# Performance work log

Hardware: AMD Instinct MI355X
Metric: run time of the kernel (lower is better)

## Reference

```python
import jax, jax.numpy as jnp
import numpy as np

COMMITMENT_COST = 0.25
ENTROPY_WEIGHT = 0.1
EPS = 1e-10


def setup_inputs() -> dict:
    key = jax.random.key(0)
    k1, k2 = jax.random.split(key)
    B, L, D, K = 8, 4096, 256, 4096
    z = jax.random.normal(k1, (B, L, D), dtype=jnp.float32)
    # torch init: uniform(-1/K, 1/K)
    codebook_weight = jax.random.uniform(k2, (K, D), dtype=jnp.float32,
                                         minval=-1.0 / K, maxval=1.0 / K)
    return {"z": z, "codebook_weight": codebook_weight}


def reference(z, codebook_weight):
    B, L, D = z.shape
    z_flat = z.reshape(-1, D)                       # [N, D]
    # squared euclidean distances: [N, K]
    d2 = (jnp.sum(z_flat ** 2, axis=1, keepdims=True)
          + jnp.sum(codebook_weight ** 2, axis=1)
          - 2.0 * z_flat @ codebook_weight.T)
    indices = jnp.argmin(d2, axis=1)                # [N]
    z_q_flat = codebook_weight[indices]             # gather [N, D]
    z_q = z_q_flat.reshape(B, L, D)

    codebook_loss = jnp.mean((z_q - jax.lax.stop_gradient(z)) ** 2)
    commitment_loss = jnp.mean((jax.lax.stop_gradient(z_q) - z) ** 2)

    probs = jax.nn.softmax(-d2, axis=1)             # [N, K]
    avg_probs = probs.mean(axis=0)                  # [K]
    entropy = -jnp.sum(avg_probs * jnp.log(avg_probs + EPS))
    entropy_loss = -entropy

    codebook_commitment_loss = codebook_loss + COMMITMENT_COST * commitment_loss
    scaled_entropy_loss = ENTROPY_WEIGHT * entropy_loss
    vq_loss = codebook_commitment_loss + scaled_entropy_loss

    # straight-through estimator
    z_q_ste = z + jax.lax.stop_gradient(z_q - z)
    indices_out = indices.reshape(B, L)
    return (z_q_ste, indices_out, vq_loss, codebook_commitment_loss, scaled_entropy_loss)
```

## Files before the change

### kernel.cpp

```cpp
#include <hip/hip_runtime.h>
#include <stdint.h>

#define NROWS 32768
#define KC 4096
#define DIM 256
#define BM 32
#define NCT 128
#define NWV 8
#define TPW 16
#define CAP 40
#define KAPPA 0.99960f
#define K2L2E 2.88539008f
#define L2E 1.44269504f

#define OUT_IDX (NROWS * DIM)
#define OUT_SCAL (OUT_IDX + NROWS)

#define WS_CNORM 0
#define WS_ZNORM 16384
#define WS_LOSS  147456
#define WS_AVGP8 147712
#define WS_FRAG  278784

typedef __bf16 bf8 __attribute__((ext_vector_type(8)));
typedef float f16v __attribute__((ext_vector_type(16)));

__device__ __forceinline__ unsigned ford(float f) {
  unsigned u = __float_as_uint(f);
  return (u & 0x80000000u) ? ~u : (u | 0x80000000u);
}

__device__ __forceinline__ float np_rownorm256(const float* __restrict__ p) {
  float h[2];
  #pragma unroll
  for (int half = 0; half < 2; ++half) {
    const float* b = p + half * 128;
    float r[8];
    #pragma unroll
    for (int j = 0; j < 8; ++j) { float v = b[j]; r[j] = __fmul_rn(v, v); }
    for (int i = 8; i < 128; i += 8) {
      #pragma unroll
      for (int j = 0; j < 8; ++j) {
        float v = b[i + j];
        r[j] = __fadd_rn(r[j], __fmul_rn(v, v));
      }
    }
    h[half] = __fadd_rn(
        __fadd_rn(__fadd_rn(r[0], r[1]), __fadd_rn(r[2], r[3])),
        __fadd_rn(__fadd_rn(r[4], r[5]), __fadd_rn(r[6], r[7])));
  }
  return __fadd_rn(h[0], h[1]);
}

__global__ void k_norms(const float* __restrict__ cbw, const float* __restrict__ z,
                        float* __restrict__ cnorm, float* __restrict__ znorm) {
  int r = blockIdx.x * 256 + threadIdx.x;
  if (r < KC) cnorm[r] = np_rownorm256(cbw + (size_t)r * DIM);
  else {
    int q = r - KC;
    if (q < NROWS) znorm[q] = np_rownorm256(z + (size_t)q * DIM);
  }
}

__global__ void k_frag(const float* __restrict__ cbw, __bf16* __restrict__ frag) {
  int idx = blockIdx.x * 256 + threadIdx.x;
  int c = idx >> 5, u = idx & 31;
  int ds = u >> 1, half = u & 1;
  int ct = c >> 5, m = c & 31;
  int lane = half * 32 + m;
  const float* src = cbw + (size_t)c * DIM + ds * 16 + half * 8;
  float4 a = *(const float4*)src;
  float4 b = *(const float4*)(src + 4);
  bf8 h;
  h[0] = (__bf16)a.x; h[1] = (__bf16)a.y; h[2] = (__bf16)a.z; h[3] = (__bf16)a.w;
  h[4] = (__bf16)b.x; h[5] = (__bf16)b.y; h[6] = (__bf16)b.z; h[7] = (__bf16)b.w;
  *(bf8*)(frag + ((size_t)(ct * 16 + ds) * 64 + lane) * 8) = h;
}

__device__ __forceinline__ float exact_d2(const float* __restrict__ zr,
                                          const float* __restrict__ cr,
                                          float rn, float cn) {
  float mm = 0.f;
  for (int d = 0; d < DIM; d += 4) {
    float4 zv = *(const float4*)(zr + d);
    float4 cv = *(const float4*)(cr + d);
    mm = __builtin_fmaf(zv.x, cv.x, mm);
    mm = __builtin_fmaf(zv.y, cv.y, mm);
    mm = __builtin_fmaf(zv.z, cv.z, mm);
    mm = __builtin_fmaf(zv.w, cv.w, mm);
  }
  return __fsub_rn(__fadd_rn(rn, cn), __fmul_rn(2.f, mm));
}

__device__ __forceinline__ void tile_mfma(const __bf16* __restrict__ Aimg,
                                          const __bf16* __restrict__ tb,
                                          int lane, f16v& acc) {
  #pragma unroll
  for (int r = 0; r < 16; ++r) acc[r] = 0.f;
  #pragma unroll
  for (int ds = 0; ds < 16; ++ds) {
    bf8 Bf = *(const bf8*)(tb + (ds * 64 + lane) * 8);
    bf8 Af = *(const bf8*)&Aimg[((size_t)ds * 64 + lane) * 8];
    acc = __builtin_amdgcn_mfma_f32_32x32x16_bf16(Af, Bf, acc, 0, 0, 0);
  }
}

__global__ __launch_bounds__(512, 4) void k_main(
    const float* __restrict__ z, const float* __restrict__ cbw,
    const float* __restrict__ cnorm, const float* __restrict__ znorm,
    const __bf16* __restrict__ frag, float* __restrict__ out,
    float* __restrict__ avgp8, double* __restrict__ losssum) {
  __shared__ __bf16 Aimg[16 * 64 * 8];
  union CP { int cand[BM][CAP]; float pcol[KC]; };
  __shared__ CP cp;
  __shared__ int ccount[BM];
  __shared__ unsigned rowmaxU[BM];
  __shared__ unsigned long long rowkey[BM];
  __shared__ float esumL[BM], invR[BM], lred[512];
  __shared__ int idxr[BM];

  const int t = threadIdx.x;
  const int lane = t & 63, wv = t >> 6;
  const int ln31 = lane & 31, lh = lane >> 5;
  const int row0 = blockIdx.x * BM;

  if (t < BM) {
    ccount[t] = 0; rowmaxU[t] = 0u; rowkey[t] = ~0ULL; esumL[t] = 0.f;
  }

  #pragma unroll
  for (int i = 0; i < 2; ++i) {
    int idx = t * 2 + i;
    int l = idx & 63, ds = idx >> 6;
    int row = l & 31, d0 = ds * 16 + (l >> 5) * 8;
    const float* src = z + (size_t)(row0 + row) * DIM + d0;
    float4 a = *(const float4*)src;
    float4 b = *(const float4*)(src + 4);
    bf8 h;
    h[0] = (__bf16)a.x; h[1] = (__bf16)a.y; h[2] = (__bf16)a.z; h[3] = (__bf16)a.w;
    h[4] = (__bf16)b.x; h[5] = (__bf16)b.y; h[6] = (__bf16)b.z; h[7] = (__bf16)b.w;
    *(bf8*)&Aimg[((size_t)ds * 64 + l) * 8] = h;
  }
  __syncthreads();

  const int ctbase = wv * TPW;

  {
    f16v acc;
    tile_mfma(Aimg, frag + (size_t)ctbase * 8192, lane, acc);
    const float cnl = cnorm[ctbase * 32 + ln31] * L2E;
    #pragma unroll
    for (int r = 0; r < 16; ++r) {
      const int row = (r & 3) + 8 * (r >> 2) + 4 * lh;
      float e = exp2f(__builtin_fmaf(acc[r], K2L2E, -cnl));
      atomicMax(&rowmaxU[row], __float_as_uint(e));
    }
  }
  __syncthreads();

  float es[16];
  #pragma unroll
  for (int i = 0; i < 16; ++i) es[i] = 0.f;

  for (int ti = 0; ti < TPW; ++ti) {
    const int ct = ctbase + ti;
    const float cnl = cnorm[ct * 32 + ln31] * L2E;

    float cr[16];
    {
      const float4* rmf = (const float4*)rowmaxU;
      float4 c0 = rmf[lh], c1 = rmf[2 + lh], c2 = rmf[4 + lh], c3 = rmf[6 + lh];
      cr[0]  = c0.x; cr[1]  = c0.y; cr[2]  = c0.z; cr[3]  = c0.w;
      cr[4]  = c1.x; cr[5]  = c1.y; cr[6]  = c1.z; cr[7]  = c1.w;
      cr[8]  = c2.x; cr[9]  = c2.y; cr[10] = c2.z; cr[11] = c2.w;
      cr[12] = c3.x; cr[13] = c3.y; cr[14] = c3.z; cr[15] = c3.w;
    }

    f16v acc;
    tile_mfma(Aimg, frag + (size_t)ct * 8192, lane, acc);

    unsigned cond = 0u;
    #pragma unroll
    for (int r = 0; r < 16; ++r) {
      float e = exp2f(__builtin_fmaf(acc[r], K2L2E, -cnl));
      es[r] += e;
      cond |= (e >= cr[r] * KAPPA) ? (1u << r) : 0u;
    }
    if (cond) {
      #pragma unroll
      for (int r = 0; r < 16; ++r) {
        if (cond & (1u << r)) {
          const int row = (r & 3) + 8 * (r >> 2) + 4 * lh;
          float e = exp2f(__builtin_fmaf(acc[r], K2L2E, -cnl));
          atomicMax(&rowmaxU[row], __float_as_uint(e));
          int slot = atomicAdd(&ccount[row], 1);
          if (slot < CAP) cp.cand[row][slot] = ct * 32 + ln31;
        }
      }
    }
  }

  #pragma unroll
  for (int r = 0; r < 16; ++r) {
    float e = es[r];
    #pragma unroll
    for (int off = 16; off > 0; off >>= 1) e += __shfl_xor(e, off);
    if (ln31 == 0) {
      const int row = (r & 3) + 8 * (r >> 2) + 4 * lh;
      atomicAdd(&esumL[row], e);
    }
  }
  __syncthreads();
  if (t < BM) invR[t] = 1.0f / esumL[t];
  __syncthreads();

  {
    int r = t & 31, q = t >> 5;
    int cnt = ccount[r];
    const float* zr = z + (size_t)(row0 + r) * DIM;
    float rn = znorm[row0 + r];
    if (cnt <= CAP) {
      for (int s = q; s < cnt; s += 16) {
        int k = cp.cand[r][s];
        float d2 = exact_d2(zr, cbw + (size_t)k * DIM, rn, cnorm[k]);
        atomicMin(&rowkey[r], (((unsigned long long)ford(d2)) << 32) | (unsigned)k);
      }
    } else {
      for (int k = q; k < KC; k += 16) {
        float d2 = exact_d2(zr, cbw + (size_t)k * DIM, rn, cnorm[k]);
        atomicMin(&rowkey[r], (((unsigned long long)ford(d2)) << 32) | (unsigned)k);
      }
    }
  }
  __syncthreads();
  if (t < BM) {
    int idx = (int)(rowkey[t] & 0xFFFFFFFFULL);
    idxr[t] = idx;
    out[OUT_IDX + row0 + t] = (float)idx;
  }
  __syncthreads();

  float lacc = 0.f;
  {
    const int col = t & 255;
    for (int r = (t >> 8); r < BM; r += 2) {
      int idx = idxr[r];
      float zq = cbw[(size_t)idx * DIM + col];
      float zv = z[(size_t)(row0 + r) * DIM + col];
      float df = __fsub_rn(zq, zv);
      out[(size_t)(row0 + r) * DIM + col] = __fadd_rn(zv, df);
      lacc += df * df;
    }
  }
  lred[t] = lacc;
  __syncthreads();
  #pragma unroll
  for (int s = 256; s > 0; s >>= 1) {
    if (t < s) lred[t] += lred[t + s];
    __syncthreads();
  }
  if (t == 0) atomicAdd(losssum, (double)lred[0]);

  float ir[16];
  #pragma unroll
  for (int r = 0; r < 16; ++r)
    ir[r] = invR[(r & 3) + 8 * (r >> 2) + 4 * lh];
  __syncthreads();

  for (int ti = 0; ti < TPW; ++ti) {
    const int ct = ctbase + ti;
    f16v acc;
    tile_mfma(Aimg, frag + (size_t)ct * 8192, lane, acc);
    const float cnl = cnorm[ct * 32 + ln31] * L2E;
    float s = 0.f;
    #pragma unroll
    for (int r = 0; r < 16; ++r) {
      float e = exp2f(__builtin_fmaf(acc[r], K2L2E, -cnl));
      s = __builtin_fmaf(e, ir[r], s);
    }
    s += __shfl_xor(s, 32);
    if (lh == 0) cp.pcol[ct * 32 + ln31] = s;
  }
  __syncthreads();
  {
    float* shadow = avgp8 + (size_t)(blockIdx.x & 7) * KC;
    #pragma unroll
    for (int i = 0; i < 8; ++i)
      atomicAdd(&shadow[t + 512 * i], cp.pcol[t + 512 * i]);
  }
}

__global__ void k_final(const float* __restrict__ avgp8,
                        const double* __restrict__ losssum,
                        float* __restrict__ out) {
  const int t = threadIdx.x;
  double part = 0.0;
  for (int k = t; k < KC; k += 256) {
    float a4 = 0.f;
    #pragma unroll
    for (int s = 0; s < 8; ++s) a4 += avgp8[s * KC + k];
    double a = (double)a4 / (double)NROWS;
    part += a * log(a + 1e-10);
  }
  __shared__ double sd[256];
  sd[t] = part;
  __syncthreads();
  for (int s = 128; s > 0; s >>= 1) {
    if (t < s) sd[t] += sd[t + s];
    __syncthreads();
  }
  if (t == 0) {
    double H = -sd[0];
    double mse = losssum[0] / (double)((size_t)NROWS * DIM);
    double ccl = 1.25 * mse;
    double sel = -0.1 * H;
    out[OUT_SCAL + 0] = (float)(ccl + sel);
    out[OUT_SCAL + 1] = (float)ccl;
    out[OUT_SCAL + 2] = (float)sel;
  }
}

extern "C" void kernel_launch(void* const* d_in, const int* in_sizes, int n_in,
                              void* d_out, int out_size, void* d_ws, size_t ws_size,
                              hipStream_t stream) {
  const float* z = (const float*)d_in[0];
  const float* cbw = (const float*)d_in[1];
  float* out = (float*)d_out;
  char* ws = (char*)d_ws;
  float* cnorm = (float*)(ws + WS_CNORM);
  float* znorm = (float*)(ws + WS_ZNORM);
  double* losssum = (double*)(ws + WS_LOSS);
  float* avgp8 = (float*)(ws + WS_AVGP8);
  __bf16* frag = (__bf16*)(ws + WS_FRAG);

  hipMemsetAsync(ws + WS_LOSS, 0, 8, stream);
  hipMemsetAsync(ws + WS_AVGP8, 0, 8 * KC * 4, stream);
  k_norms<<<(KC + NROWS) / 256, 256, 0, stream>>>(cbw, z, cnorm, znorm);
  k_frag<<<(KC * 32) / 256, 256, 0, stream>>>(cbw, frag);
  k_main<<<NROWS / BM, 512, 0, stream>>>(z, cbw, cnorm, znorm, frag, out,
                                         avgp8, losssum);
  k_final<<<1, 256, 0, stream>>>(avgp8, losssum, out);
}
```

Measured before the change: 464.5 us.

## Double-buffer codebook fragments into LDS via global_load_lds in both MFMA passes

Replaces direct global loads of B fragments inside the MFMA loops with a double-buffered LDS staging pipeline, using async global-to-LDS copies one half-tile ahead. Both the argmin/softmax-sum pass and the probability pass now run 34/32-step loops with a block-wide barrier each step. The second pass writes its column sums straight to the global shadow array with atomics instead of going through a shared buffer. The new 128KB of LDS staging forces launch bounds down from 4 to 2 blocks per CU, and the per-step barriers add synchronisation cost.

New measurement: 582.7 us. 1.25x slower.

```diff
diff --git a/kernel.cpp b/kernel.cpp
--- a/kernel.cpp
+++ b/kernel.cpp
@@ -24,6 +24,11 @@
 
 typedef __bf16 bf8 __attribute__((ext_vector_type(8)));
 typedef float f16v __attribute__((ext_vector_type(16)));
+
+#define GLOAD_LDS(g, l) \
+  __builtin_amdgcn_global_load_lds( \
+      (const __attribute__((address_space(1))) void*)(g), \
+      (__attribute__((address_space(3))) void*)(l), 16, 0, 0)
 
 __device__ __forceinline__ unsigned ford(float f) {
   unsigned u = __float_as_uint(f);
@@ -92,27 +97,24 @@
   return __fsub_rn(__fadd_rn(rn, cn), __fmul_rn(2.f, mm));
 }
 
-__device__ __forceinline__ void tile_mfma(const __bf16* __restrict__ Aimg,
-                                          const __bf16* __restrict__ tb,
-                                          int lane, f16v& acc) {
-  #pragma unroll
-  for (int r = 0; r < 16; ++r) acc[r] = 0.f;
-  #pragma unroll
-  for (int ds = 0; ds < 16; ++ds) {
-    bf8 Bf = *(const bf8*)(tb + (ds * 64 + lane) * 8);
-    bf8 Af = *(const bf8*)&Aimg[((size_t)ds * 64 + lane) * 8];
-    acc = __builtin_amdgcn_mfma_f32_32x32x16_bf16(Af, Bf, acc, 0, 0, 0);
-  }
-}
-
-__global__ __launch_bounds__(512, 4) void k_main(
+__device__ __forceinline__ void stage_half(const __bf16* __restrict__ frag,
+                                           __bf16* dst, int ct, int h, int lane) {
+  const char* g = (const char*)frag + (size_t)ct * 16384 + (size_t)h * 8192
+                  + (size_t)lane * 16;
+  char* l = (char*)dst;
+  #pragma unroll
+  for (int c = 0; c < 8; ++c)
+    GLOAD_LDS(g + c * 1024, l + c * 1024);
+}
+
+__global__ __launch_bounds__(512, 2) void k_main(
     const float* __restrict__ z, const float* __restrict__ cbw,
     const float* __restrict__ cnorm, const float* __restrict__ znorm,
     const __bf16* __restrict__ frag, float* __restrict__ out,
     float* __restrict__ avgp8, double* __restrict__ losssum) {
-  __shared__ __bf16 Aimg[16 * 64 * 8];
-  union CP { int cand[BM][CAP]; float pcol[KC]; };
-  __shared__ CP cp;
+  __shared__ __attribute__((aligned(16))) __bf16 Aimg[16 * 64 * 8];
+  __shared__ __attribute__((aligned(16))) __bf16 Bst[2][NWV][4096];
+  __shared__ int cand[BM][CAP];
   __shared__ int ccount[BM];
   __shared__ unsigned rowmaxU[BM];
   __shared__ unsigned long long rowkey[BM];
@@ -145,58 +147,77 @@
 
   const int ctbase = wv * TPW;
 
+  float es[16];
+  #pragma unroll
+  for (int i = 0; i < 16; ++i) es[i] = 0.f;
+
+#define CONSUME_HALF(bufptr, hh)                                              \
+  {                                                                           \
+    const __bf16* bs_ = (bufptr);                                             \
+    _Pragma("unroll")                                                         \
+    for (int c_ = 0; c_ < 8; ++c_) {                                          \
+      bf8 Bf = *(const bf8*)(bs_ + c_ * 512 + lane * 8);                      \
+      bf8 Af = *(const bf8*)&Aimg[((size_t)((hh) * 8 + c_) * 64 + lane) * 8]; \
+      acc = __builtin_amdgcn_mfma_f32_32x32x16_bf16(Af, Bf, acc, 0, 0, 0);    \
+    }                                                                         \
+  }
+
   {
+    stage_half(frag, &Bst[0][wv][0], ctbase, 0, lane);
+    __syncthreads();
+
+    float cr[16];
     f16v acc;
-    tile_mfma(Aimg, frag + (size_t)ctbase * 8192, lane, acc);
-    const float cnl = cnorm[ctbase * 32 + ln31] * L2E;
-    #pragma unroll
-    for (int r = 0; r < 16; ++r) {
-      const int row = (r & 3) + 8 * (r >> 2) + 4 * lh;
-      float e = exp2f(__builtin_fmaf(acc[r], K2L2E, -cnl));
-      atomicMax(&rowmaxU[row], __float_as_uint(e));
-    }
-  }
-  __syncthreads();
-
-  float es[16];
-  #pragma unroll
-  for (int i = 0; i < 16; ++i) es[i] = 0.f;
-
-  for (int ti = 0; ti < TPW; ++ti) {
-    const int ct = ctbase + ti;
-    const float cnl = cnorm[ct * 32 + ln31] * L2E;
-
-    float cr[16];
-    {
-      const float4* rmf = (const float4*)rowmaxU;
-      float4 c0 = rmf[lh], c1 = rmf[2 + lh], c2 = rmf[4 + lh], c3 = rmf[6 + lh];
-      cr[0]  = c0.x; cr[1]  = c0.y; cr[2]  = c0.z; cr[3]  = c0.w;
-      cr[4]  = c1.x; cr[5]  = c1.y; cr[6]  = c1.z; cr[7]  = c1.w;
-      cr[8]  = c2.x; cr[9]  = c2.y; cr[10] = c2.z; cr[11] = c2.w;
-      cr[12] = c3.x; cr[13] = c3.y; cr[14] = c3.z; cr[15] = c3.w;
-    }
-
-    f16v acc;
-    tile_mfma(Aimg, frag + (size_t)ct * 8192, lane, acc);
-
-    unsigned cond = 0u;
-    #pragma unroll
-    for (int r = 0; r < 16; ++r) {
-      float e = exp2f(__builtin_fmaf(acc[r], K2L2E, -cnl));
-      es[r] += e;
-      cond |= (e >= cr[r] * KAPPA) ? (1u << r) : 0u;
-    }
-    if (cond) {
-      #pragma unroll
-      for (int r = 0; r < 16; ++r) {
-        if (cond & (1u << r)) {
-          const int row = (r & 3) + 8 * (r >> 2) + 4 * lh;
-          float e = exp2f(__builtin_fmaf(acc[r], K2L2E, -cnl));
-          atomicMax(&rowmaxU[row], __float_as_uint(e));
-          int slot = atomicAdd(&ccount[row], 1);
-          if (slot < CAP) cp.cand[row][slot] = ct * 32 + ln31;
+    for (int s = 0; s < 34; ++s) {
+      {
+        int sn = (s + 1 < 34) ? (s + 1) : 33;
+        int ctn = ctbase + (sn < 2 ? 0 : ((sn - 2) >> 1));
+        stage_half(frag, &Bst[(s + 1) & 1][wv][0], ctn, sn & 1, lane);
+      }
+      if ((s & 1) == 0) {
+        #pragma unroll
+        for (int r = 0; r < 16; ++r) acc[r] = 0.f;
+        const float4* rmf = (const float4*)rowmaxU;
+        float4 c0 = rmf[lh], c1 = rmf[2 + lh], c2 = rmf[4 + lh], c3 = rmf[6 + lh];
+        cr[0]  = c0.x; cr[1]  = c0.y; cr[2]  = c0.z; cr[3]  = c0.w;
+        cr[4]  = c1.x; cr[5]  = c1.y; cr[6]  = c1.z; cr[7]  = c1.w;
+        cr[8]  = c2.x; cr[9]  = c2.y; cr[10] = c2.z; cr[11] = c2.w;
+        cr[12] = c3.x; cr[13] = c3.y; cr[14] = c3.z; cr[15] = c3.w;
+      }
+      CONSUME_HALF(&Bst[s & 1][wv][0], s & 1)
+      if (s & 1) {
+        const int ct = (s == 1) ? ctbase : (ctbase + ((s - 2) >> 1));
+        const float cnl = cnorm[ct * 32 + ln31] * L2E;
+        if (s == 1) {
+          #pragma unroll
+          for (int r = 0; r < 16; ++r) {
+            const int row = (r & 3) + 8 * (r >> 2) + 4 * lh;
+            float e = exp2f(__builtin_fmaf(acc[r], K2L2E, -cnl));
+            atomicMax(&rowmaxU[row], __float_as_uint(e));
+          }
+        } else {
+          unsigned cond = 0u;
+          #pragma unroll
+          for (int r = 0; r < 16; ++r) {
+            float e = exp2f(__builtin_fmaf(acc[r], K2L2E, -cnl));
+            es[r] += e;
+            cond |= (e >= cr[r] * KAPPA) ? (1u << r) : 0u;
+          }
+          if (cond) {
+            #pragma unroll
+            for (int r = 0; r < 16; ++r) {
+              if (cond & (1u << r)) {
+                const int row = (r & 3) + 8 * (r >> 2) + 4 * lh;
+                float e = exp2f(__builtin_fmaf(acc[r], K2L2E, -cnl));
+                atomicMax(&rowmaxU[row], __float_as_uint(e));
+                int slot = atomicAdd(&ccount[row], 1);
+                if (slot < CAP) cand[row][slot] = ct * 32 + ln31;
+              }
+            }
+          }
         }
       }
+      __syncthreads();
     }
   }
 
@@ -221,7 +242,7 @@
     float rn = znorm[row0 + r];
     if (cnt <= CAP) {
       for (int s = q; s < cnt; s += 16) {
-        int k = cp.cand[r][s];
+        int k = cand[r][s];
         float d2 = exact_d2(zr, cbw + (size_t)k * DIM, rn, cnorm[k]);
         atomicMin(&rowkey[r], (((unsigned long long)ford(d2)) << 32) | (unsigned)k);
       }
@@ -267,26 +288,35 @@
     ir[r] = invR[(r & 3) + 8 * (r >> 2) + 4 * lh];
   __syncthreads();
 
-  for (int ti = 0; ti < TPW; ++ti) {
-    const int ct = ctbase + ti;
-    f16v acc;
-    tile_mfma(Aimg, frag + (size_t)ct * 8192, lane, acc);
-    const float cnl = cnorm[ct * 32 + ln31] * L2E;
-    float s = 0.f;
-    #pragma unroll
-    for (int r = 0; r < 16; ++r) {
-      float e = exp2f(__builtin_fmaf(acc[r], K2L2E, -cnl));
-      s = __builtin_fmaf(e, ir[r], s);
-    }
-    s += __shfl_xor(s, 32);
-    if (lh == 0) cp.pcol[ct * 32 + ln31] = s;
-  }
-  __syncthreads();
   {
     float* shadow = avgp8 + (size_t)(blockIdx.x & 7) * KC;
-    #pragma unroll
-    for (int i = 0; i < 8; ++i)
-      atomicAdd(&shadow[t + 512 * i], cp.pcol[t + 512 * i]);
+    stage_half(frag, &Bst[0][wv][0], ctbase, 0, lane);
+    __syncthreads();
+    f16v acc;
+    for (int s = 0; s < 32; ++s) {
+      {
+        int sn = (s + 1 < 32) ? (s + 1) : 31;
+        stage_half(frag, &Bst[(s + 1) & 1][wv][0], ctbase + (sn >> 1), sn & 1, lane);
+      }
+      if ((s & 1) == 0) {
+        #pragma unroll
+        for (int r = 0; r < 16; ++r) acc[r] = 0.f;
+      }
+      CONSUME_HALF(&Bst[s & 1][wv][0], s & 1)
+      if (s & 1) {
+        const int ct = ctbase + (s >> 1);
+        const float cnl = cnorm[ct * 32 + ln31] * L2E;
+        float s2 = 0.f;
+        #pragma unroll
+        for (int r = 0; r < 16; ++r) {
+          float e = exp2f(__builtin_fmaf(acc[r], K2L2E, -cnl));
+          s2 = __builtin_fmaf(e, ir[r], s2);
+        }
+        s2 += __shfl_xor(s2, 32);
+        if (lh == 0) atomicAdd(&shadow[ct * 32 + ln31], s2);
+      }
+      __syncthreads();
+    }
   }
 }
 
```
